# Performance work log

Hardware: AMD Instinct MI355X
Metric: run time of the kernel (lower is better)

Reference implementation:

```python
import jax, jax.numpy as jnp
import numpy as np

B, L = 4096, 200
USER_COUNT, ITEM_COUNT, CATE_COUNT = 100000, 100000, 1000
USER_DIM, ITEM_DIM, CATE_DIM = 128, 64, 64
BN_EPS = 1e-5


def setup_inputs() -> dict:
    key = jax.random.key(0)
    ks = jax.random.split(key, 16)
    # ragged history: valid prefix of `length` items (ids >= 1), zero-padded tail
    length = jax.random.randint(ks[3], (B,), 1, L + 1)
    hist_raw = jax.random.randint(ks[2], (B, L), 1, ITEM_COUNT)
    history = jnp.where(jnp.arange(L)[None, :] < length[:, None], hist_raw, 0)
    inp = {
        "user": jax.random.randint(ks[0], (B,), 0, USER_COUNT),
        "item": jax.random.randint(ks[1], (B,), 0, ITEM_COUNT),
        "history": history,
        "length": length,
        "cate_list": jax.random.randint(ks[4], (ITEM_COUNT,), 0, CATE_COUNT),
        "user_emb_W": jax.random.normal(ks[5], (USER_COUNT, USER_DIM), jnp.float32) * 0.05,
        "item_emb_W": jax.random.normal(ks[6], (ITEM_COUNT, ITEM_DIM), jnp.float32) * 0.05,
        "cate_emb_W": jax.random.normal(ks[7], (CATE_COUNT, CATE_DIM), jnp.float32) * 0.05,
        "bn_gamma": 1.0 + 0.1 * jax.random.normal(ks[8], (384,), jnp.float32),
        "bn_beta": 0.1 * jax.random.normal(ks[9], (384,), jnp.float32),
        "W1": jax.random.normal(ks[10], (200, 384), jnp.float32) * (1.0 / np.sqrt(384)),
        "b1": jnp.zeros((200,), jnp.float32),
        "a1": jnp.full((), 0.25, jnp.float32),
        "W2": jax.random.normal(ks[11], (80, 200), jnp.float32) * (1.0 / np.sqrt(200)),
        "b2": jnp.zeros((80,), jnp.float32),
        "a2": jnp.full((), 0.25, jnp.float32),
        "W3": jax.random.normal(ks[12], (2, 80), jnp.float32) * (1.0 / np.sqrt(80)),
        "b3": jnp.zeros((2,), jnp.float32),
    }
    return inp


def _prelu(x, a):
    return jnp.where(x >= 0, x, a * x)


def reference(user, item, history, length, cate_list,
              user_emb_W, item_emb_W, cate_emb_W, bn_gamma, bn_beta,
              W1, b1, a1, W2, b2, a2, W3, b3):
    u = user_emb_W[user]                                              # [B,128]
    it = jnp.concatenate([item_emb_W[item], cate_emb_W[cate_list[item]]], -1)  # [B,128]

    # Faithful replication of get_emb's loop semantics:
    # row b uses the prefix of `history[b]` up to (and incl.) the position
    # just before the first zero; a row whose first entry is 0 halts the
    # outer loop, zeroing that row and all following rows.
    nz = history != 0                                                 # [B,L]
    prefix = jnp.concatenate(
        [jnp.ones((history.shape[0], 1), bool),
         jnp.cumprod(nz[:, 1:].astype(jnp.int32), axis=1).astype(bool)], axis=1)
    row_active = jnp.cumprod(nz[:, 0].astype(jnp.int32)).astype(bool)  # outer break
    mask = prefix & row_active[:, None]                               # [B,L]

    he = jnp.concatenate([item_emb_W[history], cate_emb_W[cate_list[history]]], -1)  # [B,L,128]
    cnt = jnp.maximum(mask.sum(-1), 1).astype(he.dtype)               # [B]
    pooled = (he * mask[..., None].astype(he.dtype)).sum(1) / cnt[:, None]  # [B,128]

    x = jnp.concatenate([u, it, pooled], -1)                          # [B,384]
    # BatchNorm1d in training mode (batch stats, biased variance)
    mean = x.mean(0)
    var = x.var(0)
    x = (x - mean) * jax.lax.rsqrt(var + BN_EPS) * bn_gamma + bn_beta
    x = _prelu(x @ W1.T + b1, a1)
    x = _prelu(x @ W2.T + b2, a2)
    x = x @ W3.T + b3
    return jax.nn.softmax(x, axis=1)
```

## Files before the change

### kernel.cpp

```cpp
#include <hip/hip_runtime.h>
#include <hip/hip_bf16.h>

#define B_SZ 4096
#define L_SZ 200

typedef __bf16 bf16x8 __attribute__((ext_vector_type(8)));
typedef float  f32x4  __attribute__((ext_vector_type(4)));

static __device__ inline unsigned short bfbits(float f) {
    return __builtin_bit_cast(unsigned short, (__bf16)f);
}

__global__ void k_init(int* __restrict__ first_bad, float* __restrict__ acc) {
    int t = threadIdx.x;
    if (t == 0) first_bad[0] = B_SZ;
    if (t < 768) acc[t] = 0.f;
}

__global__ void k_firstbad(const int* __restrict__ history, int* __restrict__ first_bad) {
    int b = threadIdx.x + blockIdx.x * blockDim.x;
    if (b < B_SZ && history[(size_t)b * L_SZ] == 0) atomicMin(first_bad, b);
}

__global__ __launch_bounds__(64) void k_wfrag(const float* __restrict__ W1,
                                              const float* __restrict__ W2,
                                              ushort* __restrict__ W1f,
                                              ushort* __restrict__ W2f) {
    const int bid = blockIdx.x, lane = threadIdx.x;
    const int nr = lane & 15, quad = lane >> 4;
    ushort v[8];
    if (bid < 156) {
        const int oT = bid / 12, kS = bid % 12;
        const int o = oT * 16 + nr;
        #pragma unroll
        for (int j = 0; j < 8; ++j) {
            int k = kS * 32 + quad * 8 + j;
            v[j] = (o < 200) ? bfbits(W1[(size_t)o * 384 + k]) : (ushort)0;
        }
        ushort* dst = W1f + ((size_t)bid * 64 + lane) * 8;
        *(ushort4*)(dst)     = make_ushort4(v[0], v[1], v[2], v[3]);
        *(ushort4*)(dst + 4) = make_ushort4(v[4], v[5], v[6], v[7]);
    } else {
        const int idx = bid - 156;
        const int oT = idx / 7, kS = idx % 7;
        const int o = oT * 16 + nr;
        #pragma unroll
        for (int j = 0; j < 8; ++j) {
            int k = kS * 32 + quad * 8 + j;
            v[j] = (k < 200) ? bfbits(W2[(size_t)o * 200 + k]) : (ushort)0;
        }
        ushort* dst = W2f + ((size_t)idx * 64 + lane) * 8;
        *(ushort4*)(dst)     = make_ushort4(v[0], v[1], v[2], v[3]);
        *(ushort4*)(dst + 4) = make_ushort4(v[4], v[5], v[6], v[7]);
    }
}

__global__ __launch_bounds__(256) void k_pool(
    const int* __restrict__ user, const int* __restrict__ item,
    const int* __restrict__ history, const int* __restrict__ cate_list,
    const float* __restrict__ user_W, const float* __restrict__ item_W,
    const float* __restrict__ cate_W, const int* __restrict__ first_bad,
    float* __restrict__ x)
{
    const int b = blockIdx.x;
    const int tid = threadIdx.x;
    __shared__ int sh_item[L_SZ];
    __shared__ int sh_cid[L_SZ];
    __shared__ int s_fz;
    __shared__ __align__(16) float red[8][128];
    if (tid == 0) s_fz = L_SZ;
    __syncthreads();
    if (tid < L_SZ) {
        int h = history[(size_t)b * L_SZ + tid];
        sh_item[tid] = h;
        if (tid >= 1 && h == 0) atomicMin(&s_fz, tid);
        sh_cid[tid] = cate_list[h];
    }
    __syncthreads();
    const bool active = (b < first_bad[0]);
    const int valid = active ? s_fz : 0;
    const float inv_cnt = 1.0f / (float)max(valid, 1);

    const int group = tid >> 5, lane = tid & 31;
    const int sub = lane >> 4, q = lane & 15;
    const float* tab = (sub == 0) ? item_W : cate_W;
    const int*   ids = (sub == 0) ? sh_item : sh_cid;
    float4 acc = make_float4(0.f, 0.f, 0.f, 0.f);
    int l = group;
    for (; l + 8 < valid; l += 16) {
        int id0 = ids[l], id1 = ids[l + 8];
        float4 v0 = ((const float4*)(tab + (size_t)id0 * 64))[q];
        float4 v1 = ((const float4*)(tab + (size_t)id1 * 64))[q];
        acc.x += v0.x + v1.x; acc.y += v0.y + v1.y;
        acc.z += v0.z + v1.z; acc.w += v0.w + v1.w;
    }
    if (l < valid) {
        int id = ids[l];
        float4 v = ((const float4*)(tab + (size_t)id * 64))[q];
        acc.x += v.x; acc.y += v.y; acc.z += v.z; acc.w += v.w;
    }
    *((float4*)&red[group][lane * 4]) = acc;
    __syncthreads();

    float* xrow = x + (size_t)b * 384;
    if (tid < 128) {
        float s = 0.f;
        #pragma unroll
        for (int g = 0; g < 8; ++g) s += red[g][tid];
        xrow[256 + tid] = s * inv_cnt;
        xrow[tid] = user_W[(size_t)user[b] * 128 + tid];
    } else if (tid < 192) {
        int f = tid - 128;
        xrow[128 + f] = item_W[(size_t)item[b] * 64 + f];
    } else {
        int f = tid - 192;
        xrow[192 + f] = cate_W[(size_t)cate_list[item[b]] * 64 + f];
    }
}

__global__ __launch_bounds__(384) void k_bnstats(const float* __restrict__ x,
                                                 float* __restrict__ acc) {
    const int f = threadIdx.x;
    const int r0 = blockIdx.x * 32;
    float s = 0.f, s2 = 0.f;
    for (int r = r0; r < r0 + 32; ++r) {
        float v = x[(size_t)r * 384 + f];
        s += v; s2 += v * v;
    }
    atomicAdd(&acc[f], s);
    atomicAdd(&acc[384 + f], s2);
}

__global__ void k_bnfinal(const float* __restrict__ acc,
                          const float* __restrict__ gamma,
                          const float* __restrict__ beta,
                          float* __restrict__ A, float* __restrict__ C) {
    int f = threadIdx.x;
    if (f < 384) {
        const float inv_b = 1.0f / (float)B_SZ;
        float mean = acc[f] * inv_b;
        float var  = acc[384 + f] * inv_b - mean * mean;
        float a = gamma[f] * rsqrtf(var + 1e-5f);
        A[f] = a;
        C[f] = beta[f] - mean * a;
    }
}

#define XS_STRIDE 392
#define H1_STRIDE 232

__global__ __launch_bounds__(256) void k_mlp(
    const float* __restrict__ x, const float* __restrict__ A, const float* __restrict__ C,
    const ushort* __restrict__ W1f, const float* __restrict__ b1, const float* __restrict__ a1p,
    const ushort* __restrict__ W2f, const float* __restrict__ b2, const float* __restrict__ a2p,
    const float* __restrict__ W3, const float* __restrict__ b3,
    float* __restrict__ out)
{
    const int r0 = blockIdx.x * 16;
    const int tid = threadIdx.x;
    const int lane = tid & 63, wv = tid >> 6;
    const int nr = lane & 15, quad = lane >> 4;

    __shared__ __align__(16) __bf16 xs[16 * XS_STRIDE];
    __shared__ __align__(16) __bf16 h1s[16 * H1_STRIDE];
    __shared__ __align__(16) float  h2s[16][84];

    {
        const float4* xg = (const float4*)(x + (size_t)r0 * 384);
        const float4* A4 = (const float4*)A;
        const float4* C4 = (const float4*)C;
        for (int e = tid; e < 16 * 96; e += 256) {
            int rr = e / 96, f4 = e - rr * 96;
            float4 v = xg[e], a = A4[f4], c = C4[f4];
            ushort4 p = make_ushort4(bfbits(v.x * a.x + c.x), bfbits(v.y * a.y + c.y),
                                     bfbits(v.z * a.z + c.z), bfbits(v.w * a.w + c.w));
            *(ushort4*)&xs[rr * XS_STRIDE + f4 * 4] = p;
        }
        if (tid < 192) {
            int rr = tid / 12, c4 = tid - rr * 12;
            *(uint*)((char*)&h1s[rr * H1_STRIDE] + 400 + c4 * 4) = 0u;
        }
    }
    __syncthreads();

    const float a1 = a1p[0], a2 = a2p[0];

    {
        f32x4 acc[4];
        #pragma unroll
        for (int i = 0; i < 4; ++i) {
            int o = (wv + 4 * i) * 16 + nr;
            float bias = (wv + 4 * i < 13 && o < 200) ? b1[o] : 0.f;
            acc[i] = (f32x4){bias, bias, bias, bias};
        }
        for (int kS = 0; kS < 12; ++kS) {
            bf16x8 af = *(const bf16x8*)&xs[nr * XS_STRIDE + kS * 32 + quad * 8];
            bf16x8 bfr[4];
            #pragma unroll
            for (int i = 0; i < 4; ++i)
                if (wv + 4 * i < 13)
                    bfr[i] = *(const bf16x8*)(W1f + (((size_t)(wv + 4 * i) * 12 + kS) * 64 + lane) * 8);
            #pragma unroll
            for (int i = 0; i < 4; ++i)
                if (wv + 4 * i < 13)
                    acc[i] = __builtin_amdgcn_mfma_f32_16x16x32_bf16(af, bfr[i], acc[i], 0, 0, 0);
        }
        #pragma unroll
        for (int i = 0; i < 4; ++i) {
            if (wv + 4 * i < 13) {
                int o = (wv + 4 * i) * 16 + nr;
                if (o < 208) {
                    #pragma unroll
                    for (int r = 0; r < 4; ++r) {
                        float s = acc[i][r];
                        s = (s >= 0.f) ? s : a1 * s;
                        h1s[(quad * 4 + r) * H1_STRIDE + o] = (__bf16)s;
                    }
                }
            }
        }
    }
    __syncthreads();

    {
        f32x4 acc[2];
        #pragma unroll
        for (int i = 0; i < 2; ++i) {
            int oT = wv + 4 * i;
            float bias = (oT < 5) ? b2[oT * 16 + nr] : 0.f;
            acc[i] = (f32x4){bias, bias, bias, bias};
        }
        for (int kS = 0; kS < 7; ++kS) {
            bf16x8 af = *(const bf16x8*)&h1s[nr * H1_STRIDE + kS * 32 + quad * 8];
            bf16x8 bfr[2];
            #pragma unroll
            for (int i = 0; i < 2; ++i)
                if (wv + 4 * i < 5)
                    bfr[i] = *(const bf16x8*)(W2f + (((size_t)(wv + 4 * i) * 7 + kS) * 64 + lane) * 8);
            #pragma unroll
            for (int i = 0; i < 2; ++i)
                if (wv + 4 * i < 5)
                    acc[i] = __builtin_amdgcn_mfma_f32_16x16x32_bf16(af, bfr[i], acc[i], 0, 0, 0);
        }
        #pragma unroll
        for (int i = 0; i < 2; ++i) {
            if (wv + 4 * i < 5) {
                int o = (wv + 4 * i) * 16 + nr;
                #pragma unroll
                for (int r = 0; r < 4; ++r) {
                    float s = acc[i][r];
                    h2s[quad * 4 + r][o] = (s >= 0.f) ? s : a2 * s;
                }
            }
        }
    }
    __syncthreads();

    if (tid < 16) {
        float l0 = b3[0], l1 = b3[1];
        #pragma unroll 8
        for (int f = 0; f < 80; ++f) {
            float h = h2s[tid][f];
            l0 += h * W3[f];
            l1 += h * W3[80 + f];
        }
        float m = fmaxf(l0, l1);
        float e0 = expf(l0 - m), e1 = expf(l1 - m);
        float inv = 1.0f / (e0 + e1);
        out[(size_t)(r0 + tid) * 2 + 0] = e0 * inv;
        out[(size_t)(r0 + tid) * 2 + 1] = e1 * inv;
    }
}

extern "C" void kernel_launch(void* const* d_in, const int* in_sizes, int n_in,
                              void* d_out, int out_size, void* d_ws, size_t ws_size,
                              hipStream_t stream) {
    const int*   user      = (const int*)  d_in[0];
    const int*   item      = (const int*)  d_in[1];
    const int*   history   = (const int*)  d_in[2];
    const int*   cate_list = (const int*)  d_in[4];
    const float* user_W    = (const float*)d_in[5];
    const float* item_W    = (const float*)d_in[6];
    const float* cate_W    = (const float*)d_in[7];
    const float* gamma     = (const float*)d_in[8];
    const float* beta      = (const float*)d_in[9];
    const float* W1        = (const float*)d_in[10];
    const float* b1        = (const float*)d_in[11];
    const float* a1        = (const float*)d_in[12];
    const float* W2        = (const float*)d_in[13];
    const float* b2        = (const float*)d_in[14];
    const float* a2        = (const float*)d_in[15];
    const float* W3        = (const float*)d_in[16];
    const float* b3        = (const float*)d_in[17];
    float* out = (float*)d_out;

    int*   first_bad = (int*)d_ws;
    float* acc = (float*)d_ws + 16;
    float* A   = acc + 768;
    float* C   = A + 384;
    float* x   = C + 384;
    ushort* W1f = (ushort*)(x + (size_t)B_SZ * 384);
    ushort* W2f = W1f + (size_t)156 * 64 * 8;

    hipLaunchKernelGGL(k_init,     dim3(1),    dim3(768), 0, stream, first_bad, acc);
    hipLaunchKernelGGL(k_firstbad, dim3(16),   dim3(256), 0, stream, history, first_bad);
    hipLaunchKernelGGL(k_wfrag,    dim3(191),  dim3(64),  0, stream, W1, W2, W1f, W2f);
    hipLaunchKernelGGL(k_pool,     dim3(B_SZ), dim3(256), 0, stream,
                       user, item, history, cate_list, user_W, item_W, cate_W,
                       first_bad, x);
    hipLaunchKernelGGL(k_bnstats,  dim3(128),  dim3(384), 0, stream, x, acc);
    hipLaunchKernelGGL(k_bnfinal,  dim3(1),    dim3(384), 0, stream, acc, gamma, beta, A, C);
    hipLaunchKernelGGL(k_mlp,      dim3(B_SZ/16), dim3(256), 0, stream,
                       x, A, C, W1f, b1, a1, W2f, b2, a2, W3, b3, out);
}
```

Before: 182.9 us.

## Store features in bf16, split MLP into per-layer kernels, merge prep kernels

Feature rows are now written as bf16 instead of fp32, halving the intermediate traffic read by the BN-stats and layer-1 kernels. The init and first-zero kernels are merged into one single-block reduction, and the BN finalize step is folded into the layer-1 kernel. The fused MLP is replaced by a layer-1 kernel with one 16x16 output tile per wave across 832 blocks and a layer-2/3 kernel that finishes the tiny final layer with cross-lane shuffles. This trades launch count and occupancy for an extra bf16 round trip of the hidden activations and a lower-precision BN statistics input.

```diff
diff --git a/kernel.cpp b/kernel.cpp
--- a/kernel.cpp
+++ b/kernel.cpp
@@ -10,16 +10,26 @@
 static __device__ inline unsigned short bfbits(float f) {
     return __builtin_bit_cast(unsigned short, (__bf16)f);
 }
-
-__global__ void k_init(int* __restrict__ first_bad, float* __restrict__ acc) {
-    int t = threadIdx.x;
-    if (t == 0) first_bad[0] = B_SZ;
-    if (t < 768) acc[t] = 0.f;
-}
-
-__global__ void k_firstbad(const int* __restrict__ history, int* __restrict__ first_bad) {
-    int b = threadIdx.x + blockIdx.x * blockDim.x;
-    if (b < B_SZ && history[(size_t)b * L_SZ] == 0) atomicMin(first_bad, b);
+static __device__ inline float bf2f(unsigned short u) {
+    return __builtin_bit_cast(float, (unsigned int)u << 16);
+}
+
+__global__ __launch_bounds__(1024) void k_prep(const int* __restrict__ history,
+                                               int* __restrict__ first_bad,
+                                               float* __restrict__ acc) {
+    const int tid = threadIdx.x;
+    if (tid < 768) acc[tid] = 0.f;
+    int m = B_SZ;
+    for (int b = tid; b < B_SZ; b += 1024)
+        if (history[(size_t)b * L_SZ] == 0) m = min(m, b);
+    __shared__ int red[1024];
+    red[tid] = m;
+    __syncthreads();
+    for (int s = 512; s > 0; s >>= 1) {
+        if (tid < s) red[tid] = min(red[tid], red[tid + s]);
+        __syncthreads();
+    }
+    if (tid == 0) first_bad[0] = red[0];
 }
 
 __global__ __launch_bounds__(64) void k_wfrag(const float* __restrict__ W1,
@@ -60,7 +70,7 @@
     const int* __restrict__ history, const int* __restrict__ cate_list,
     const float* __restrict__ user_W, const float* __restrict__ item_W,
     const float* __restrict__ cate_W, const int* __restrict__ first_bad,
-    float* __restrict__ x)
+    ushort* __restrict__ xb)
 {
     const int b = blockIdx.x;
     const int tid = threadIdx.x;
@@ -102,173 +112,156 @@
     *((float4*)&red[group][lane * 4]) = acc;
     __syncthreads();
 
-    float* xrow = x + (size_t)b * 384;
+    ushort* xrow = xb + (size_t)b * 384;
     if (tid < 128) {
         float s = 0.f;
         #pragma unroll
         for (int g = 0; g < 8; ++g) s += red[g][tid];
-        xrow[256 + tid] = s * inv_cnt;
-        xrow[tid] = user_W[(size_t)user[b] * 128 + tid];
+        xrow[256 + tid] = bfbits(s * inv_cnt);
+        xrow[tid] = bfbits(user_W[(size_t)user[b] * 128 + tid]);
     } else if (tid < 192) {
         int f = tid - 128;
-        xrow[128 + f] = item_W[(size_t)item[b] * 64 + f];
+        xrow[128 + f] = bfbits(item_W[(size_t)item[b] * 64 + f]);
     } else {
         int f = tid - 192;
-        xrow[192 + f] = cate_W[(size_t)cate_list[item[b]] * 64 + f];
-    }
-}
-
-__global__ __launch_bounds__(384) void k_bnstats(const float* __restrict__ x,
+        xrow[192 + f] = bfbits(cate_W[(size_t)cate_list[item[b]] * 64 + f]);
+    }
+}
+
+__global__ __launch_bounds__(384) void k_bnstats(const ushort* __restrict__ xb,
                                                  float* __restrict__ acc) {
     const int f = threadIdx.x;
     const int r0 = blockIdx.x * 32;
     float s = 0.f, s2 = 0.f;
     for (int r = r0; r < r0 + 32; ++r) {
-        float v = x[(size_t)r * 384 + f];
+        float v = bf2f(xb[(size_t)r * 384 + f]);
         s += v; s2 += v * v;
     }
     atomicAdd(&acc[f], s);
     atomicAdd(&acc[384 + f], s2);
 }
 
-__global__ void k_bnfinal(const float* __restrict__ acc,
-                          const float* __restrict__ gamma,
-                          const float* __restrict__ beta,
-                          float* __restrict__ A, float* __restrict__ C) {
-    int f = threadIdx.x;
-    if (f < 384) {
+__global__ __launch_bounds__(256) void k_l1(
+    const ushort* __restrict__ xb, const float* __restrict__ accv,
+    const float* __restrict__ gamma, const float* __restrict__ beta,
+    const ushort* __restrict__ W1f, const float* __restrict__ b1,
+    const float* __restrict__ a1p, ushort* __restrict__ h1b)
+{
+    __shared__ float As[384], Cs[384];
+    const int tid = threadIdx.x;
+    for (int f = tid; f < 384; f += 256) {
         const float inv_b = 1.0f / (float)B_SZ;
-        float mean = acc[f] * inv_b;
-        float var  = acc[384 + f] * inv_b - mean * mean;
+        float mean = accv[f] * inv_b;
+        float var  = accv[384 + f] * inv_b - mean * mean;
         float a = gamma[f] * rsqrtf(var + 1e-5f);
-        A[f] = a;
-        C[f] = beta[f] - mean * a;
-    }
-}
-
-#define XS_STRIDE 392
-#define H1_STRIDE 232
-
-__global__ __launch_bounds__(256) void k_mlp(
-    const float* __restrict__ x, const float* __restrict__ A, const float* __restrict__ C,
-    const ushort* __restrict__ W1f, const float* __restrict__ b1, const float* __restrict__ a1p,
-    const ushort* __restrict__ W2f, const float* __restrict__ b2, const float* __restrict__ a2p,
+        As[f] = a;
+        Cs[f] = beta[f] - mean * a;
+    }
+    __syncthreads();
+
+    const int lane = tid & 63, wv = tid >> 6;
+    const int nr = lane & 15, quad = lane >> 4;
+    const int wid = blockIdx.x * 4 + wv;
+    const int mT = wid / 13, oT = wid - mT * 13;
+    const int o = oT * 16 + nr;
+    const float a1 = a1p[0];
+
+    float bias = (o < 200) ? b1[o] : 0.f;
+    f32x4 acc = {bias, bias, bias, bias};
+    const ushort* xrow = xb + (size_t)(mT * 16 + nr) * 384;
+
+    for (int kS = 0; kS < 12; ++kS) {
+        const int kc = kS * 32 + quad * 8;
+        bf16x8 a8 = *(const bf16x8*)(xrow + kc);
+        float4 A0 = *(const float4*)&As[kc],     A1 = *(const float4*)&As[kc + 4];
+        float4 C0 = *(const float4*)&Cs[kc],     C1 = *(const float4*)&Cs[kc + 4];
+        bf16x8 w;
+        w[0] = (__bf16)((float)a8[0] * A0.x + C0.x);
+        w[1] = (__bf16)((float)a8[1] * A0.y + C0.y);
+        w[2] = (__bf16)((float)a8[2] * A0.z + C0.z);
+        w[3] = (__bf16)((float)a8[3] * A0.w + C0.w);
+        w[4] = (__bf16)((float)a8[4] * A1.x + C1.x);
+        w[5] = (__bf16)((float)a8[5] * A1.y + C1.y);
+        w[6] = (__bf16)((float)a8[6] * A1.z + C1.z);
+        w[7] = (__bf16)((float)a8[7] * A1.w + C1.w);
+        bf16x8 bfr = *(const bf16x8*)(W1f + (((size_t)oT * 12 + kS) * 64 + lane) * 8);
+        acc = __builtin_amdgcn_mfma_f32_16x16x32_bf16(w, bfr, acc, 0, 0, 0);
+    }
+
+    #pragma unroll
+    for (int r = 0; r < 4; ++r) {
+        int row = mT * 16 + quad * 4 + r;
+        float s = acc[r];
+        s = (s >= 0.f) ? s : a1 * s;
+        h1b[(size_t)row * 224 + o] = bfbits(s);
+        if (oT == 12) h1b[(size_t)row * 224 + o + 16] = 0;
+    }
+}
+
+__global__ __launch_bounds__(256) void k_l23(
+    const ushort* __restrict__ h1b, const ushort* __restrict__ W2f,
+    const float* __restrict__ b2, const float* __restrict__ a2p,
     const float* __restrict__ W3, const float* __restrict__ b3,
     float* __restrict__ out)
 {
-    const int r0 = blockIdx.x * 16;
     const int tid = threadIdx.x;
     const int lane = tid & 63, wv = tid >> 6;
     const int nr = lane & 15, quad = lane >> 4;
-
-    __shared__ __align__(16) __bf16 xs[16 * XS_STRIDE];
-    __shared__ __align__(16) __bf16 h1s[16 * H1_STRIDE];
-    __shared__ __align__(16) float  h2s[16][84];
-
-    {
-        const float4* xg = (const float4*)(x + (size_t)r0 * 384);
-        const float4* A4 = (const float4*)A;
-        const float4* C4 = (const float4*)C;
-        for (int e = tid; e < 16 * 96; e += 256) {
-            int rr = e / 96, f4 = e - rr * 96;
-            float4 v = xg[e], a = A4[f4], c = C4[f4];
-            ushort4 p = make_ushort4(bfbits(v.x * a.x + c.x), bfbits(v.y * a.y + c.y),
-                                     bfbits(v.z * a.z + c.z), bfbits(v.w * a.w + c.w));
-            *(ushort4*)&xs[rr * XS_STRIDE + f4 * 4] = p;
-        }
-        if (tid < 192) {
-            int rr = tid / 12, c4 = tid - rr * 12;
-            *(uint*)((char*)&h1s[rr * H1_STRIDE] + 400 + c4 * 4) = 0u;
-        }
-    }
-    __syncthreads();
-
-    const float a1 = a1p[0], a2 = a2p[0];
-
-    {
-        f32x4 acc[4];
-        #pragma unroll
-        for (int i = 0; i < 4; ++i) {
-            int o = (wv + 4 * i) * 16 + nr;
-            float bias = (wv + 4 * i < 13 && o < 200) ? b1[o] : 0.f;
-            acc[i] = (f32x4){bias, bias, bias, bias};
-        }
-        for (int kS = 0; kS < 12; ++kS) {
-            bf16x8 af = *(const bf16x8*)&xs[nr * XS_STRIDE + kS * 32 + quad * 8];
-            bf16x8 bfr[4];
-            #pragma unroll
-            for (int i = 0; i < 4; ++i)
-                if (wv + 4 * i < 13)
-                    bfr[i] = *(const bf16x8*)(W1f + (((size_t)(wv + 4 * i) * 12 + kS) * 64 + lane) * 8);
-            #pragma unroll
-            for (int i = 0; i < 4; ++i)
-                if (wv + 4 * i < 13)
-                    acc[i] = __builtin_amdgcn_mfma_f32_16x16x32_bf16(af, bfr[i], acc[i], 0, 0, 0);
-        }
-        #pragma unroll
-        for (int i = 0; i < 4; ++i) {
-            if (wv + 4 * i < 13) {
-                int o = (wv + 4 * i) * 16 + nr;
-                if (o < 208) {
-                    #pragma unroll
-                    for (int r = 0; r < 4; ++r) {
-                        float s = acc[i][r];
-                        s = (s >= 0.f) ? s : a1 * s;
-                        h1s[(quad * 4 + r) * H1_STRIDE + o] = (__bf16)s;
-                    }
-                }
-            }
-        }
-    }
-    __syncthreads();
-
-    {
-        f32x4 acc[2];
-        #pragma unroll
-        for (int i = 0; i < 2; ++i) {
-            int oT = wv + 4 * i;
-            float bias = (oT < 5) ? b2[oT * 16 + nr] : 0.f;
-            acc[i] = (f32x4){bias, bias, bias, bias};
-        }
-        for (int kS = 0; kS < 7; ++kS) {
-            bf16x8 af = *(const bf16x8*)&h1s[nr * H1_STRIDE + kS * 32 + quad * 8];
-            bf16x8 bfr[2];
-            #pragma unroll
-            for (int i = 0; i < 2; ++i)
-                if (wv + 4 * i < 5)
-                    bfr[i] = *(const bf16x8*)(W2f + (((size_t)(wv + 4 * i) * 7 + kS) * 64 + lane) * 8);
-            #pragma unroll
-            for (int i = 0; i < 2; ++i)
-                if (wv + 4 * i < 5)
-                    acc[i] = __builtin_amdgcn_mfma_f32_16x16x32_bf16(af, bfr[i], acc[i], 0, 0, 0);
-        }
-        #pragma unroll
-        for (int i = 0; i < 2; ++i) {
-            if (wv + 4 * i < 5) {
-                int o = (wv + 4 * i) * 16 + nr;
-                #pragma unroll
-                for (int r = 0; r < 4; ++r) {
-                    float s = acc[i][r];
-                    h2s[quad * 4 + r][o] = (s >= 0.f) ? s : a2 * s;
-                }
-            }
-        }
-    }
-    __syncthreads();
-
-    if (tid < 16) {
-        float l0 = b3[0], l1 = b3[1];
-        #pragma unroll 8
-        for (int f = 0; f < 80; ++f) {
-            float h = h2s[tid][f];
-            l0 += h * W3[f];
-            l1 += h * W3[80 + f];
-        }
-        float m = fmaxf(l0, l1);
-        float e0 = expf(l0 - m), e1 = expf(l1 - m);
-        float inv = 1.0f / (e0 + e1);
-        out[(size_t)(r0 + tid) * 2 + 0] = e0 * inv;
-        out[(size_t)(r0 + tid) * 2 + 1] = e1 * inv;
+    const int mT = blockIdx.x * 4 + wv;
+    const float a2 = a2p[0];
+
+    f32x4 acc[5];
+    #pragma unroll
+    for (int i = 0; i < 5; ++i) {
+        float bb = b2[i * 16 + nr];
+        acc[i] = (f32x4){bb, bb, bb, bb};
+    }
+    const ushort* hrow = h1b + (size_t)(mT * 16 + nr) * 224;
+    for (int kS = 0; kS < 7; ++kS) {
+        bf16x8 a8 = *(const bf16x8*)(hrow + kS * 32 + quad * 8);
+        #pragma unroll
+        for (int i = 0; i < 5; ++i) {
+            bf16x8 bfr = *(const bf16x8*)(W2f + (((size_t)i * 7 + kS) * 64 + lane) * 8);
+            acc[i] = __builtin_amdgcn_mfma_f32_16x16x32_bf16(a8, bfr, acc[i], 0, 0, 0);
+        }
+    }
+
+    float w0[5], w1[5];
+    #pragma unroll
+    for (int i = 0; i < 5; ++i) {
+        w0[i] = W3[i * 16 + nr];
+        w1[i] = W3[80 + i * 16 + nr];
+    }
+    f32x4 p0 = {0.f, 0.f, 0.f, 0.f}, p1 = {0.f, 0.f, 0.f, 0.f};
+    #pragma unroll
+    for (int i = 0; i < 5; ++i) {
+        #pragma unroll
+        for (int r = 0; r < 4; ++r) {
+            float s = acc[i][r];
+            s = (s >= 0.f) ? s : a2 * s;
+            p0[r] += s * w0[i];
+            p1[r] += s * w1[i];
+        }
+    }
+    #pragma unroll
+    for (int m = 1; m < 16; m <<= 1) {
+        #pragma unroll
+        for (int r = 0; r < 4; ++r) {
+            p0[r] += __shfl_xor(p0[r], m, 64);
+            p1[r] += __shfl_xor(p1[r], m, 64);
+        }
+    }
+    if (nr == 0) {
+        float B0 = b3[0], B1 = b3[1];
+        #pragma unroll
+        for (int r = 0; r < 4; ++r) {
+            float l0 = p0[r] + B0, l1 = p1[r] + B1;
+            float mx = fmaxf(l0, l1);
+            float e0 = expf(l0 - mx), e1 = expf(l1 - mx);
+            float inv = 1.0f / (e0 + e1);
+            int row = mT * 16 + quad * 4 + r;
+            *(float2*)(out + (size_t)row * 2) = make_float2(e0 * inv, e1 * inv);
+        }
     }
 }
 
@@ -294,22 +287,22 @@
     const float* b3        = (const float*)d_in[17];
     float* out = (float*)d_out;
 
-    int*   first_bad = (int*)d_ws;
-    float* acc = (float*)d_ws + 16;
-    float* A   = acc + 768;
-    float* C   = A + 384;
-    float* x   = C + 384;
-    ushort* W1f = (ushort*)(x + (size_t)B_SZ * 384);
-    ushort* W2f = W1f + (size_t)156 * 64 * 8;
-
-    hipLaunchKernelGGL(k_init,     dim3(1),    dim3(768), 0, stream, first_bad, acc);
-    hipLaunchKernelGGL(k_firstbad, dim3(16),   dim3(256), 0, stream, history, first_bad);
-    hipLaunchKernelGGL(k_wfrag,    dim3(191),  dim3(64),  0, stream, W1, W2, W1f, W2f);
-    hipLaunchKernelGGL(k_pool,     dim3(B_SZ), dim3(256), 0, stream,
+    char* ws = (char*)d_ws;
+    int*    first_bad = (int*)   ws;
+    float*  acc       = (float*)(ws + 64);
+    ushort* xb        = (ushort*)(ws + 3200);
+    ushort* h1b       = (ushort*)(ws + 3148928);
+    ushort* W1f       = (ushort*)(ws + 4983936);
+    ushort* W2f       = (ushort*)(ws + 5143680);
+
+    hipLaunchKernelGGL(k_prep,    dim3(1),    dim3(1024), 0, stream, history, first_bad, acc);
+    hipLaunchKernelGGL(k_wfrag,   dim3(191),  dim3(64),   0, stream, W1, W2, W1f, W2f);
+    hipLaunchKernelGGL(k_pool,    dim3(B_SZ), dim3(256),  0, stream,
                        user, item, history, cate_list, user_W, item_W, cate_W,
-                       first_bad, x);
-    hipLaunchKernelGGL(k_bnstats,  dim3(128),  dim3(384), 0, stream, x, acc);
-    hipLaunchKernelGGL(k_bnfinal,  dim3(1),    dim3(384), 0, stream, acc, gamma, beta, A, C);
-    hipLaunchKernelGGL(k_mlp,      dim3(B_SZ/16), dim3(256), 0, stream,
-                       x, A, C, W1f, b1, a1, W2f, b2, a2, W3, b3, out);
-}
+                       first_bad, xb);
+    hipLaunchKernelGGL(k_bnstats, dim3(128),  dim3(384),  0, stream, xb, acc);
+    hipLaunchKernelGGL(k_l1,      dim3(832),  dim3(256),  0, stream,
+                       xb, acc, gamma, beta, W1f, b1, a1, h1b);
+    hipLaunchKernelGGL(k_l23,     dim3(64),   dim3(256),  0, stream,
+                       h1b, W2f, b2, a2, W3, b3, out);
+}
```

Result: no change. 182.1 us (median of 2 runs) (-0.4%).
